# Kernel optimization log

Measured on AMD Instinct MI355X. Metric: run time of the kernel, lower is better.

The kernel has to match this reference:

```python
import jax, jax.numpy as jnp
import numpy as np

CURV = 0.9            # geoopt PoincareBall(0.9)
SQRT_C = CURV ** 0.5
MIN_NORM = 1e-15
PROJ_EPS = 4e-3       # geoopt float32 boundary eps
ATANH_EPS = 1e-7
COS_EPS = 1e-8        # torch.cosine_similarity eps


def _norm(x):
    return jnp.sqrt(jnp.maximum(jnp.sum(x * x, axis=-1, keepdims=True), MIN_NORM * MIN_NORM))


def _project(x):
    # project onto ball of radius (1-eps)/sqrt(c)
    n = jnp.maximum(_norm(x), MIN_NORM)
    maxnorm = (1.0 - PROJ_EPS) / SQRT_C
    return jnp.where(n > maxnorm, x / n * maxnorm, x)


def expmap0(u):
    n = jnp.maximum(_norm(u), MIN_NORM)
    gamma = jnp.tanh(SQRT_C * n) * u / (SQRT_C * n)
    return _project(gamma)


def mobius_add(x, y):
    c = CURV
    x2 = jnp.sum(x * x, axis=-1, keepdims=True)
    y2 = jnp.sum(y * y, axis=-1, keepdims=True)
    xy = jnp.sum(x * y, axis=-1, keepdims=True)
    num = (1.0 + 2.0 * c * xy + c * y2) * x + (1.0 - c * x2) * y
    den = 1.0 + 2.0 * c * xy + c * c * x2 * y2
    return num / jnp.maximum(den, MIN_NORM)


def pdist(x, y):
    # dist(x,y) = 2/sqrt(c) * artanh(sqrt(c) * ||(-x) (+) y||)
    d = mobius_add(-x, y)
    n = _norm(d)[..., 0]
    z = jnp.clip(SQRT_C * n, -1.0 + ATANH_EPS, 1.0 - ATANH_EPS)
    return 2.0 / SQRT_C * jnp.arctanh(z)


def cos_sim(a, b):
    na = jnp.maximum(jnp.sqrt(jnp.sum(a * a, axis=-1)), COS_EPS)
    nb = jnp.maximum(jnp.sqrt(jnp.sum(b * b, axis=-1)), COS_EPS)
    return jnp.sum(a * b, axis=-1) / (na * nb)


def setup_inputs() -> dict:
    key = jax.random.key(0)
    ks = jax.random.split(key, 11)
    B, L, Ls, C, Lc, H, R = 4, 512, 128, 20, 128, 768, 512
    s = 0.02  # keep projected embeddings in a realistic range
    return {
        "text_out": jax.random.normal(ks[0], (B, L, H), jnp.float32),
        "summary_out": jax.random.normal(ks[1], (B, Ls, H), jnp.float32),
        "candidate_out": jax.random.normal(ks[2], (B, C, Lc, H), jnp.float32),
        "W_d": jax.random.normal(ks[3], (H, R), jnp.float32) * s,
        "W_s": jax.random.normal(ks[4], (H, R), jnp.float32) * s,
        "W_c": jax.random.normal(ks[5], (H, R), jnp.float32) * s,
        "W_p": jax.random.normal(ks[6], (R, R), jnp.float32) * s,
        "conv_w1": jax.random.normal(ks[7], (1, H, R), jnp.float32) * s,
        "conv_b1": jax.random.normal(ks[8], (R,), jnp.float32) * s,
        "conv_w2": jax.random.normal(ks[9], (2, H, R), jnp.float32) * s,
        "conv_b2": jax.random.normal(ks[10], (R,), jnp.float32) * s,
    }


def _forward(text_out, summary_out, candidate_out, W_d, W_s, W_c, W_p,
             conv_w1, conv_b1, conv_w2, conv_b2):
    # --- document ---
    doc_emb = expmap0(text_out[:, 0, :] @ W_d)                       # [B,R]

    # NGramers (max_gram=2, eval mode so dropout is identity)
    x = text_out[:, 1:-1, :]                                         # [B,L-2,H]
    y1 = jax.nn.relu(jnp.einsum('blh,hr->blr', x, conv_w1[0]) + conv_b1)
    y2 = jax.nn.relu(jnp.einsum('blh,hr->blr', x[:, :-1], conv_w2[0])
                     + jnp.einsum('blh,hr->blr', x[:, 1:], conv_w2[1]) + conv_b2)
    gram = jnp.concatenate([y1, y2], axis=1)                         # [B,2L-5,R]

    doc_word_emb = expmap0(jnp.einsum('blr,rk->blk', gram, W_p))     # [B,T,R]
    doc_inter = 1.0 / pdist(doc_word_emb, doc_emb[:, None, :])       # [B,T]

    # --- summary ---
    summary_emb = expmap0(jnp.max(summary_out, axis=1) @ W_s)        # [B,R]
    summary_score = -pdist(summary_emb, doc_emb) ** 2                # [B]
    sum_inter = 1.0 / pdist(doc_word_emb, summary_emb[:, None, :])   # [B,T]
    summary_score = summary_score + cos_sim(doc_inter, sum_inter)    # [B]

    # --- candidates ---
    cand_emb = expmap0(jnp.einsum('bch,hr->bcr', jnp.max(candidate_out, axis=2), W_c))  # [B,C,R]
    score = -pdist(cand_emb, doc_emb[:, None, :]) ** 2               # [B,C]
    cand_inter = 1.0 / pdist(doc_word_emb[:, None, :, :], cand_emb[:, :, None, :])      # [B,C,T]
    score = score + cos_sim(doc_inter[:, None, :], cand_inter)       # [B,C]
    return score, summary_score


def reference(text_out, summary_out, candidate_out, W_d, W_s, W_c, W_p,
              conv_w1, conv_b1, conv_w2, conv_b2):
    return _forward(text_out, summary_out, candidate_out, W_d, W_s, W_c, W_p,
                    conv_w1, conv_b1, conv_w2, conv_b2)
```

## Files before the change

### kernel.cpp

```cpp
#include <hip/hip_runtime.h>
#include <math.h>

#define SQRTC  0.94868329805051381f
#define MAXN   (0.996f/SQRTC)
#define OME_CLIP (1.0f - 0.996f*0.996f)
#define TWO_OVER_SQRTC 2.1081851067789197f

typedef unsigned short u16;
typedef __attribute__((ext_vector_type(8))) short bf8;
typedef __attribute__((ext_vector_type(4))) float f4;

__device__ __forceinline__ u16 f2bf(float f){
    union { float f; unsigned int i; } v; v.f = f;
    unsigned int x = v.i;
    unsigned int lsb = (x >> 16) & 1u;
    x += 0x7fffu + lsb;
    return (u16)(x >> 16);
}
__device__ __forceinline__ float bf2f(u16 u){
    union { unsigned int i; float f; } v; v.i = ((unsigned int)u) << 16; return v.f;
}

__device__ __forceinline__ void gload16(void* lds, const void* g){
    __builtin_amdgcn_global_load_lds(
        (const __attribute__((address_space(1))) unsigned int*)g,
        (__attribute__((address_space(3))) unsigned int*)lds,
        16, 0, 0);
}

__device__ __forceinline__ float pdist_stable(float ome_x, float ome_y, float t){
    float u = 1.0f - ome_x, v = 1.0f - ome_y;
    float den = fmaxf(1.0f - 1.8f*t + u*v, 1e-15f);
    float q = ome_x*ome_y/den;
    q = fminf(fmaxf(q, 2.0e-7f), 1.0f);
    float z = sqrtf(fmaxf(1.0f - q, 0.0f));
    float at = 0.5f * logf((1.0f+z)*(1.0f+z)/q);
    return TWO_OVER_SQRTC * at;
}

__device__ __forceinline__ void expmap_scale_ome(float sum, float* fout, float* omeout){
    float nraw = sqrtf(fmaxf(sum, 1e-30f));
    float n = fmaxf(nraw, 1e-15f);
    float sn = SQRTC*n;
    float th = tanhf(sn);
    float factor = th/sn;
    float gn = factor*nraw;
    if (gn > MAXN){ *fout = factor*(MAXN/gn); *omeout = OME_CLIP; }
    else { *fout = factor; *omeout = fmaxf((1.0f-th)*(1.0f+th), 1e-12f); }
}

__global__ __launch_bounds__(256)
void k_stage1(const float* __restrict__ summ, const float* __restrict__ cand,
              const float* __restrict__ text,
              const float* __restrict__ w1, const float* __restrict__ w2,
              const float* __restrict__ wp,
              float* __restrict__ smax, float* __restrict__ cmax,
              u16* __restrict__ textb, u16* __restrict__ w1t,
              u16* __restrict__ w2t, u16* __restrict__ wpt)
{
    __shared__ float shm[1056];
    int bx = blockIdx.x;
    int t = threadIdx.x;
    if (bx < 1008){
        int row = bx / 12, ht = bx - row*12;
        int lane = t & 63, lg = t >> 6;
        int h = ht*64 + lane;
        const float* in = (row < 4) ? (summ + (long long)row*128*768)
                                    : (cand + (long long)(row-4)*128*768);
        const float* p = in + (long long)(lg*32)*768 + h;
        float m = -INFINITY;
        #pragma unroll 8
        for (int l = 0; l < 32; l++) m = fmaxf(m, p[l*768]);
        shm[t] = m; __syncthreads();
        if (t < 64){
            float mm = fmaxf(fmaxf(shm[t], shm[t+64]), fmaxf(shm[t+128], shm[t+192]));
            if (row < 4) smax[row*768 + h] = mm;
            else cmax[(row-4)*768 + h] = mm;
        }
        return;
    }
    int pb = bx - 1008;
    if (pb < 768){
        int base = pb*2048 + t*8;
        float4 a = *(const float4*)(text + base);
        float4 b = *(const float4*)(text + base + 4);
        *(ushort4*)(textb + base)     = make_ushort4(f2bf(a.x), f2bf(a.y), f2bf(a.z), f2bf(a.w));
        *(ushort4*)(textb + base + 4) = make_ushort4(f2bf(b.x), f2bf(b.y), f2bf(b.z), f2bf(b.w));
        return;
    }
    int j = pb - 768;
    const float* in; u16* outp; int K;
    if (j < 384){ in = w1; outp = w1t; K = 768; }
    else if (j < 1152){ j -= 384; in = w2; outp = w2t; K = 1536; }
    else { j -= 1152; in = wp; outp = wpt; K = 512; }
    const int N = 512, ntile = N/32;
    int k0 = (j/ntile)*32, n0 = (j - (j/ntile)*ntile)*32;
    int tx = t & 31, ty = t >> 5;
    #pragma unroll
    for (int i = 0; i < 4; i++)
        shm[(ty*4+i)*33 + tx] = in[(long long)(k0 + ty*4 + i)*N + n0 + tx];
    __syncthreads();
    #pragma unroll
    for (int i = 0; i < 4; i++)
        outp[(long long)(n0 + ty*4 + i)*K + k0 + tx] = f2bf(shm[tx*33 + ty*4+i]);
}

__global__ __launch_bounds__(256)
void k_stage2(const u16* __restrict__ textb,
              const u16* __restrict__ w1t, const u16* __restrict__ w2t,
              const float* __restrict__ cb1, const float* __restrict__ cb2,
              const float* __restrict__ text,
              const float* __restrict__ smax, const float* __restrict__ cmax,
              const float* __restrict__ W_d, const float* __restrict__ W_s,
              const float* __restrict__ W_c,
              u16* __restrict__ gram, float* __restrict__ emb_all)
{
    __shared__ char smem[16384];
    int bx = blockIdx.x;
    int t = threadIdx.x;
    if (bx < 512){
        u16* As = (u16*)smem;
        u16* Bs = (u16*)(smem + 8192);
        int xx = bx & 63, yy = bx >> 6;
        int job = xx & 1;
        int m0 = (xx >> 1) * 64;
        int n0 = yy * 64;
        int K   = job ? 1536 : 768;
        int M   = job ? 2036 : 2040;
        int rpb = job ? 509 : 510;
        int ob  = job ? 510 : 0;
        const u16* Bt = job ? w2t : w1t;
        const float* bias = job ? cb2 : cb1;

        int r0 = t >> 3;
        int co = (((t & 7) ^ (r0 & 7)) << 3);

        int gm0 = m0 + r0;      if (gm0 >= M) gm0 = M - 1;
        int gm1 = m0 + r0 + 32; if (gm1 >= M) gm1 = M - 1;
        int ab0 = gm0 / rpb, al0 = gm0 - ab0*rpb;
        int ab1 = gm1 / rpb, al1 = gm1 - ab1*rpb;
        const u16* a0 = textb + (long long)ab0*393216 + (long long)(al0+1)*768 + co;
        const u16* a1 = textb + (long long)ab1*393216 + (long long)(al1+1)*768 + co;
        const u16* bp0 = Bt + (long long)(n0 + r0)*K      + co;
        const u16* bp1 = Bt + (long long)(n0 + r0 + 32)*K + co;
        u16* lA0 = As + t*8;
        u16* lA1 = As + (256 + t)*8;
        u16* lB0 = Bs + t*8;
        u16* lB1 = Bs + (256 + t)*8;

        int lane = t & 63, wv = t >> 6;
        int fm = lane & 15, fq = lane >> 4;
        int arow = wv*16 + fm;
        int aswz = arow & 7, bswz = fm & 7;
        int aoff0 = arow*64 + ((fq     ^ aswz) << 3);
        int aoff1 = arow*64 + (((4+fq) ^ aswz) << 3);
        int boff0 = ((fq     ^ bswz) << 3);
        int boff1 = (((4+fq) ^ bswz) << 3);

        f4 acc0 = {0,0,0,0}, acc1 = {0,0,0,0}, acc2 = {0,0,0,0}, acc3 = {0,0,0,0};
        for (int k0 = 0; k0 < K; k0 += 64){
            gload16(lA0, a0 + k0);
            gload16(lA1, a1 + k0);
            gload16(lB0, bp0 + k0);
            gload16(lB1, bp1 + k0);
            __syncthreads();
            bf8 af0 = *(const bf8*)(As + aoff0);
            bf8 af1 = *(const bf8*)(As + aoff1);
            bf8 b00 = *(const bf8*)(Bs + (fm   )*64 + boff0);
            bf8 b10 = *(const bf8*)(Bs + (16+fm)*64 + boff0);
            bf8 b20 = *(const bf8*)(Bs + (32+fm)*64 + boff0);
            bf8 b30 = *(const bf8*)(Bs + (48+fm)*64 + boff0);
            bf8 b01 = *(const bf8*)(Bs + (fm   )*64 + boff1);
            bf8 b11 = *(const bf8*)(Bs + (16+fm)*64 + boff1);
            bf8 b21 = *(const bf8*)(Bs + (32+fm)*64 + boff1);
            bf8 b31 = *(const bf8*)(Bs + (48+fm)*64 + boff1);
            acc0 = __builtin_amdgcn_mfma_f32_16x16x32_bf16(af0, b00, acc0, 0, 0, 0);
            acc1 = __builtin_amdgcn_mfma_f32_16x16x32_bf16(af0, b10, acc1, 0, 0, 0);
            acc2 = __builtin_amdgcn_mfma_f32_16x16x32_bf16(af0, b20, acc2, 0, 0, 0);
            acc3 = __builtin_amdgcn_mfma_f32_16x16x32_bf16(af0, b30, acc3, 0, 0, 0);
            acc0 = __builtin_amdgcn_mfma_f32_16x16x32_bf16(af1, b01, acc0, 0, 0, 0);
            acc1 = __builtin_amdgcn_mfma_f32_16x16x32_bf16(af1, b11, acc1, 0, 0, 0);
            acc2 = __builtin_amdgcn_mfma_f32_16x16x32_bf16(af1, b21, acc2, 0, 0, 0);
            acc3 = __builtin_amdgcn_mfma_f32_16x16x32_bf16(af1, b31, acc3, 0, 0, 0);
            __syncthreads();
        }
        int col = n0 + fm;
        float bv0 = bias[col], bv1 = bias[col+16], bv2 = bias[col+32], bv3 = bias[col+48];
        #pragma unroll
        for (int i = 0; i < 4; i++){
            int row = m0 + wv*16 + fq*4 + i;
            if (row >= M) continue;
            int b = row/rpb, l = row - b*rpb;
            long long orow = (long long)b*1019 + ob + l;
            u16* gp = gram + orow*512;
            gp[col]      = f2bf(fmaxf(acc0[i] + bv0, 0.f));
            gp[col + 16] = f2bf(fmaxf(acc1[i] + bv1, 0.f));
            gp[col + 32] = f2bf(fmaxf(acc2[i] + bv2, 0.f));
            gp[col + 48] = f2bf(fmaxf(acc3[i] + bv3, 0.f));
        }
        return;
    }
    {
        int eb = bx - 512;
        int row = eb >> 3, nt = eb & 7;
        float* a   = (float*)smem;
        float* red = (float*)smem + 768;
        const float* A; const float* W;
        if (row < 4){ A = text + (long long)row*512*768; W = W_d; }
        else if (row < 8){ A = smax + (long long)(row-4)*768; W = W_s; }
        else { A = cmax + (long long)(row-8)*768; W = W_c; }
        for (int k = t; k < 768; k += 256) a[k] = A[k];
        __syncthreads();
        int lane = t & 63, kg = t >> 6;
        int col = nt*64 + lane;
        const float* Wp = W + (long long)(kg*192)*512 + col;
        float acc = 0.f;
        #pragma unroll 8
        for (int k = 0; k < 192; k++) acc += a[kg*192 + k] * Wp[k*512];
        red[t] = acc; __syncthreads();
        if (t < 64) emb_all[(long long)row*512 + col] = red[t] + red[t+64] + red[t+128] + red[t+192];
    }
}

__global__ __launch_bounds__(256)
void k_stage3(const u16* __restrict__ gram, const u16* __restrict__ wpt,
              u16* __restrict__ dwe_b,
              float* __restrict__ emb_all, float* __restrict__ ome_all,
              u16* __restrict__ emb_b)
{
    __shared__ char smem[16384];
    int bx = blockIdx.x;
    int t = threadIdx.x;
    if (bx < 512){
        u16* As = (u16*)smem;
        u16* Bs = (u16*)(smem + 8192);
        const int K = 512, M = 4076;
        int m0 = (bx >> 3) * 64;
        int n0 = (bx & 7) * 64;

        int r0 = t >> 3;
        int co = (((t & 7) ^ (r0 & 7)) << 3);
        int gm0 = m0 + r0;      if (gm0 >= M) gm0 = M - 1;
        int gm1 = m0 + r0 + 32; if (gm1 >= M) gm1 = M - 1;
        const u16* a0 = gram + (long long)gm0*512 + co;
        const u16* a1 = gram + (long long)gm1*512 + co;
        const u16* bp0 = wpt + (long long)(n0 + r0)*K      + co;
        const u16* bp1 = wpt + (long long)(n0 + r0 + 32)*K + co;
        u16* lA0 = As + t*8;
        u16* lA1 = As + (256 + t)*8;
        u16* lB0 = Bs + t*8;
        u16* lB1 = Bs + (256 + t)*8;

        int lane = t & 63, wv = t >> 6;
        int fm = lane & 15, fq = lane >> 4;
        int arow = wv*16 + fm;
        int aswz = arow & 7, bswz = fm & 7;
        int aoff0 = arow*64 + ((fq     ^ aswz) << 3);
        int aoff1 = arow*64 + (((4+fq) ^ aswz) << 3);
        int boff0 = ((fq     ^ bswz) << 3);
        int boff1 = (((4+fq) ^ bswz) << 3);

        f4 acc0 = {0,0,0,0}, acc1 = {0,0,0,0}, acc2 = {0,0,0,0}, acc3 = {0,0,0,0};
        for (int k0 = 0; k0 < K; k0 += 64){
            gload16(lA0, a0 + k0);
            gload16(lA1, a1 + k0);
            gload16(lB0, bp0 + k0);
            gload16(lB1, bp1 + k0);
            __syncthreads();
            bf8 af0 = *(const bf8*)(As + aoff0);
            bf8 af1 = *(const bf8*)(As + aoff1);
            bf8 b00 = *(const bf8*)(Bs + (fm   )*64 + boff0);
            bf8 b10 = *(const bf8*)(Bs + (16+fm)*64 + boff0);
            bf8 b20 = *(const bf8*)(Bs + (32+fm)*64 + boff0);
            bf8 b30 = *(const bf8*)(Bs + (48+fm)*64 + boff0);
            bf8 b01 = *(const bf8*)(Bs + (fm   )*64 + boff1);
            bf8 b11 = *(const bf8*)(Bs + (16+fm)*64 + boff1);
            bf8 b21 = *(const bf8*)(Bs + (32+fm)*64 + boff1);
            bf8 b31 = *(const bf8*)(Bs + (48+fm)*64 + boff1);
            acc0 = __builtin_amdgcn_mfma_f32_16x16x32_bf16(af0, b00, acc0, 0, 0, 0);
            acc1 = __builtin_amdgcn_mfma_f32_16x16x32_bf16(af0, b10, acc1, 0, 0, 0);
            acc2 = __builtin_amdgcn_mfma_f32_16x16x32_bf16(af0, b20, acc2, 0, 0, 0);
            acc3 = __builtin_amdgcn_mfma_f32_16x16x32_bf16(af0, b30, acc3, 0, 0, 0);
            acc0 = __builtin_amdgcn_mfma_f32_16x16x32_bf16(af1, b01, acc0, 0, 0, 0);
            acc1 = __builtin_amdgcn_mfma_f32_16x16x32_bf16(af1, b11, acc1, 0, 0, 0);
            acc2 = __builtin_amdgcn_mfma_f32_16x16x32_bf16(af1, b21, acc2, 0, 0, 0);
            acc3 = __builtin_amdgcn_mfma_f32_16x16x32_bf16(af1, b31, acc3, 0, 0, 0);
            __syncthreads();
        }
        int col = n0 + fm;
        #pragma unroll
        for (int i = 0; i < 4; i++){
            int row = m0 + wv*16 + fq*4 + i;
            if (row >= M) continue;
            u16* dp = dwe_b + (long long)row*512;
            dp[col]      = f2bf(acc0[i]);
            dp[col + 16] = f2bf(acc1[i]);
            dp[col + 32] = f2bf(acc2[i]);
            dp[col + 48] = f2bf(acc3[i]);
        }
        return;
    }
    {
        float* red = (float*)smem;
        int row = bx - 512;
        float* X = emb_all + (long long)row*512;
        float2 u = *(float2*)(X + t*2);
        red[t] = u.x*u.x + u.y*u.y; __syncthreads();
        for (int s = 128; s > 0; s >>= 1){ if (t < s) red[t] += red[t+s]; __syncthreads(); }
        float f, ome;
        expmap_scale_ome(red[0], &f, &ome);
        float sx = u.x*f, sy = u.y*f;
        *(float2*)(X + t*2) = make_float2(sx, sy);
        u16* Xb = emb_b + (long long)row*512;
        Xb[t*2]   = f2bf(sx);
        Xb[t*2+1] = f2bf(sy);
        if (t == 0) ome_all[row] = ome;
    }
}

__global__ __launch_bounds__(256)
void k_dots_mfma(const u16* __restrict__ dwe_b, const u16* __restrict__ emb_b,
                 const float* __restrict__ ome_all,
                 float* __restrict__ doc_inter, float* __restrict__ sum_inter,
                 float* __restrict__ cand_inter)
{
    __shared__ u16 As[64][32];
    __shared__ u16 Bs[32][32];
    __shared__ float ssp[64][4];
    __shared__ float ssl[64];
    __shared__ float oyl[22];
    int bx = blockIdx.x;
    int b  = bx >> 4;
    int m0 = (bx & 15) * 64;
    int t = threadIdx.x;
    int sra = t >> 2, ska = (t & 3) << 3;
    const u16* Arow = (m0 + sra < 1019) ? (dwe_b + (long long)(b*1019 + m0 + sra)*512) : nullptr;
    const u16* Brow = nullptr;
    if (t < 128){
        int n = t >> 2;
        if (n < 22){
            int ei = (n == 0) ? b : (n == 1) ? 4 + b : 8 + b*20 + (n - 2);
            Brow = emb_b + (long long)ei*512;
        }
    }
    if (t < 22) oyl[t] = ome_all[(t == 0) ? b : (t == 1) ? 4 + b : 8 + b*20 + (t - 2)];
    int lane = t & 63, wv = t >> 6;
    int fm = lane & 15, fq = lane >> 4;
    f4 acc0 = {0,0,0,0}, acc1 = {0,0,0,0};
    float ssq = 0.f;
    for (int k0 = 0; k0 < 512; k0 += 32){
        bf8 av = {};
        if (Arow) av = *(const bf8*)(Arow + k0 + ska);
        *(bf8*)&As[sra][ska] = av;
        if (t < 128){
            bf8 bv = {};
            if (Brow) bv = *(const bf8*)(Brow + k0 + ((t & 3) << 3));
            *(bf8*)&Bs[t >> 2][(t & 3) << 3] = bv;
        }
        #pragma unroll
        for (int j = 0; j < 8; j++){ float x = bf2f(((u16*)&av)[j]); ssq += x*x; }
        __syncthreads();
        bf8 af = *(const bf8*)&As[wv*16 + fm][fq*8];
        bf8 b0 = *(const bf8*)&Bs[fm][fq*8];
        bf8 b1 = *(const bf8*)&Bs[16 + fm][fq*8];
        acc0 = __builtin_amdgcn_mfma_f32_16x16x32_bf16(af, b0, acc0, 0, 0, 0);
        acc1 = __builtin_amdgcn_mfma_f32_16x16x32_bf16(af, b1, acc1, 0, 0, 0);
        __syncthreads();
    }
    ssp[sra][t & 3] = ssq; __syncthreads();
    if (t < 64) ssl[t] = ssp[t][0] + ssp[t][1] + ssp[t][2] + ssp[t][3];
    __syncthreads();
    #pragma unroll
    for (int i = 0; i < 4; i++){
        int rtile = wv*16 + fq*4 + i;
        int row = m0 + rtile;
        if (row >= 1019) continue;
        float f, ox;
        expmap_scale_ome(ssl[rtile], &f, &ox);
        long long grow = (long long)b*1019 + row;
        #pragma unroll
        for (int g = 0; g < 2; g++){
            int c = g*16 + fm;
            if (c >= 22) continue;
            float s = (g ? acc1[i] : acc0[i]) * f;
            float dist = pdist_stable(ox, oyl[c], s);
            float inv = 1.0f/fmaxf(dist, 1e-12f);
            if (c == 0) doc_inter[grow] = inv;
            else if (c == 1) sum_inter[grow] = inv;
            else cand_inter[((long long)(b*20 + (c - 2)))*1019 + row] = inv;
        }
    }
}

__global__ __launch_bounds__(256)
void k_final(const float* __restrict__ doc_inter, const float* __restrict__ sum_inter,
             const float* __restrict__ cand_inter,
             const float* __restrict__ emb_all, const float* __restrict__ ome_all,
             float* __restrict__ out)
{
    __shared__ float r0[256], r1[256], r2[256], r3[256];
    int j = blockIdx.x, t = threadIdx.x;
    int b; const float *a, *bb; int xi, yi; int outIdx;
    if (j < 80){
        b = j/20;
        a  = doc_inter + b*1019;
        bb = cand_inter + (long long)j*1019;
        xi = 8 + j; yi = b;
        outIdx = j;
    } else {
        b = j - 80;
        a  = doc_inter + b*1019;
        bb = sum_inter + b*1019;
        xi = 4 + b; yi = b;
        outIdx = 80 + b;
    }
    const float* xe = emb_all + (long long)xi*512;
    const float* ye = emb_all + (long long)yi*512;
    float ox = ome_all[xi], oy = ome_all[yi];
    float saa = 0.f, sbb = 0.f, sab = 0.f, st = 0.f;
    for (int l = t; l < 1019; l += 256){ float av = a[l], bv = bb[l]; saa += av*av; sbb += bv*bv; sab += av*bv; }
    for (int k = t; k < 512; k += 256) st += xe[k]*ye[k];
    r0[t] = saa; r1[t] = sbb; r2[t] = sab; r3[t] = st; __syncthreads();
    for (int s = 128; s > 0; s >>= 1){
        if (t < s){ r0[t] += r0[t+s]; r1[t] += r1[t+s]; r2[t] += r2[t+s]; r3[t] += r3[t+s]; }
        __syncthreads();
    }
    if (t == 0){
        float na = fmaxf(sqrtf(r0[0]), 1e-8f);
        float nb = fmaxf(sqrtf(r1[0]), 1e-8f);
        float cosv = r2[0] / (na*nb);
        float pd = pdist_stable(ox, oy, r3[0]);
        out[outIdx] = -pd*pd + cosv;
    }
}

extern "C" void kernel_launch(void* const* d_in, const int* in_sizes, int n_in,
                              void* d_out, int out_size, void* d_ws, size_t ws_size,
                              hipStream_t stream) {
    const float* text = (const float*)d_in[0];
    const float* summ = (const float*)d_in[1];
    const float* cand = (const float*)d_in[2];
    const float* W_d  = (const float*)d_in[3];
    const float* W_s  = (const float*)d_in[4];
    const float* W_c  = (const float*)d_in[5];
    const float* W_p  = (const float*)d_in[6];
    const float* cw1  = (const float*)d_in[7];
    const float* cb1  = (const float*)d_in[8];
    const float* cw2  = (const float*)d_in[9];
    const float* cb2  = (const float*)d_in[10];
    float* out = (float*)d_out;

    const int B = 4, C = 20, H = 768;

    char* base = (char*)d_ws;
    size_t off = 0;
    auto allocF = [&](size_t n)->float*{ float* p = (float*)(base + off); off += ((n*4) + 255) & ~(size_t)255; return p; };
    auto allocU = [&](size_t n)->u16*{ u16* p = (u16*)(base + off); off += ((n*2) + 255) & ~(size_t)255; return p; };

    float* smax = allocF(B*H);
    float* cmax = allocF(B*C*H);
    float* emb_all = allocF(88*512);
    float* ome_all = allocF(88);
    u16* emb_b = allocU(88*512);
    u16* textb = allocU(4*512*768);
    u16* w1t   = allocU(512*768);
    u16* w2t   = allocU(512*1536);
    u16* wpt   = allocU(512*512);
    u16* gram  = allocU(4076*512);
    u16* dwe_b = allocU(4076*512);
    float* doc_inter = allocF(4076);
    float* sum_inter = allocF(4076);
    float* cand_inter= allocF(B*C*1019);

    k_stage1<<<3184, 256, 0, stream>>>(summ, cand, text, cw1, cw2, W_p,
                                       smax, cmax, textb, w1t, w2t, wpt);

    k_stage2<<<1216, 256, 0, stream>>>(textb, w1t, w2t, cb1, cb2,
                                       text, smax, cmax, W_d, W_s, W_c,
                                       gram, emb_all);

    k_stage3<<<600, 256, 0, stream>>>(gram, wpt, dwe_b, emb_all, ome_all, emb_b);

    k_dots_mfma<<<64, 256, 0, stream>>>(dwe_b, emb_b, ome_all,
                                        doc_inter, sum_inter, cand_inter);

    k_final<<<84, 256, 0, stream>>>(doc_inter, sum_inter, cand_inter,
                                    emb_all, ome_all, out);
}
```

Baseline: 150.5 us.

## Vectorize max-pool loads and rework dots kernel into single-wave LDS-free blocks

```diff
diff --git a/kernel.cpp b/kernel.cpp
--- a/kernel.cpp
+++ b/kernel.cpp
@@ -61,25 +61,34 @@
     __shared__ float shm[1056];
     int bx = blockIdx.x;
     int t = threadIdx.x;
-    if (bx < 1008){
-        int row = bx / 12, ht = bx - row*12;
-        int lane = t & 63, lg = t >> 6;
-        int h = ht*64 + lane;
+    if (bx < 252){
+        int row = bx / 3, hc = bx - row*3;
+        int w = t >> 6, lane = t & 63;
         const float* in = (row < 4) ? (summ + (long long)row*128*768)
                                     : (cand + (long long)(row-4)*128*768);
-        const float* p = in + (long long)(lg*32)*768 + h;
-        float m = -INFINITY;
+        const float* p = in + (long long)(w*32)*768 + hc*256 + lane*4;
+        float4 m = make_float4(-INFINITY,-INFINITY,-INFINITY,-INFINITY);
         #pragma unroll 8
-        for (int l = 0; l < 32; l++) m = fmaxf(m, p[l*768]);
-        shm[t] = m; __syncthreads();
+        for (int l = 0; l < 32; l++){
+            float4 v = *(const float4*)(p + (long long)l*768);
+            m.x = fmaxf(m.x, v.x); m.y = fmaxf(m.y, v.y);
+            m.z = fmaxf(m.z, v.z); m.w = fmaxf(m.w, v.w);
+        }
+        float4* sm4 = (float4*)shm;
+        sm4[w*64 + lane] = m; __syncthreads();
         if (t < 64){
-            float mm = fmaxf(fmaxf(shm[t], shm[t+64]), fmaxf(shm[t+128], shm[t+192]));
-            if (row < 4) smax[row*768 + h] = mm;
-            else cmax[(row-4)*768 + h] = mm;
+            float4 a = sm4[t], b4 = sm4[64+t], c4 = sm4[128+t], d4 = sm4[192+t];
+            float4 r;
+            r.x = fmaxf(fmaxf(a.x,b4.x), fmaxf(c4.x,d4.x));
+            r.y = fmaxf(fmaxf(a.y,b4.y), fmaxf(c4.y,d4.y));
+            r.z = fmaxf(fmaxf(a.z,b4.z), fmaxf(c4.z,d4.z));
+            r.w = fmaxf(fmaxf(a.w,b4.w), fmaxf(c4.w,d4.w));
+            float* outp = (row < 4) ? (smax + row*768) : (cmax + (row-4)*768);
+            *(float4*)(outp + hc*256 + t*4) = r;
         }
         return;
     }
-    int pb = bx - 1008;
+    int pb = bx - 252;
     if (pb < 768){
         int base = pb*2048 + t*8;
         float4 a = *(const float4*)(text + base);
@@ -318,76 +327,66 @@
     }
 }
 
-__global__ __launch_bounds__(256)
+__global__ __launch_bounds__(64)
 void k_dots_mfma(const u16* __restrict__ dwe_b, const u16* __restrict__ emb_b,
                  const float* __restrict__ ome_all,
                  float* __restrict__ doc_inter, float* __restrict__ sum_inter,
                  float* __restrict__ cand_inter)
 {
-    __shared__ u16 As[64][32];
-    __shared__ u16 Bs[32][32];
-    __shared__ float ssp[64][4];
-    __shared__ float ssl[64];
-    __shared__ float oyl[22];
     int bx = blockIdx.x;
-    int b  = bx >> 4;
-    int m0 = (bx & 15) * 64;
+    int b  = bx >> 6;
+    int m0 = (bx & 63) * 16;
     int t = threadIdx.x;
-    int sra = t >> 2, ska = (t & 3) << 3;
-    const u16* Arow = (m0 + sra < 1019) ? (dwe_b + (long long)(b*1019 + m0 + sra)*512) : nullptr;
-    const u16* Brow = nullptr;
-    if (t < 128){
-        int n = t >> 2;
-        if (n < 22){
-            int ei = (n == 0) ? b : (n == 1) ? 4 + b : 8 + b*20 + (n - 2);
-            Brow = emb_b + (long long)ei*512;
-        }
-    }
-    if (t < 22) oyl[t] = ome_all[(t == 0) ? b : (t == 1) ? 4 + b : 8 + b*20 + (t - 2)];
-    int lane = t & 63, wv = t >> 6;
-    int fm = lane & 15, fq = lane >> 4;
+    int fm = t & 15, fq = t >> 4;
+
+    int arow = m0 + fm; if (arow > 1018) arow = 1018;
+    const u16* Ap = dwe_b + ((long long)(b*1019 + arow))*512 + fq*8;
+
+    int n1 = 16 + fm; if (n1 > 21) n1 = 21;
+    int e0 = (fm == 0) ? b : (fm == 1) ? 4 + b : 8 + b*20 + (fm - 2);
+    int e1 = 8 + b*20 + (n1 - 2);
+    const u16* B0 = emb_b + (long long)e0*512 + fq*8;
+    const u16* B1 = emb_b + (long long)e1*512 + fq*8;
+    float oy0 = ome_all[e0];
+    float oy1 = ome_all[e1];
+
     f4 acc0 = {0,0,0,0}, acc1 = {0,0,0,0};
     float ssq = 0.f;
+    #pragma unroll 4
     for (int k0 = 0; k0 < 512; k0 += 32){
-        bf8 av = {};
-        if (Arow) av = *(const bf8*)(Arow + k0 + ska);
-        *(bf8*)&As[sra][ska] = av;
-        if (t < 128){
-            bf8 bv = {};
-            if (Brow) bv = *(const bf8*)(Brow + k0 + ((t & 3) << 3));
-            *(bf8*)&Bs[t >> 2][(t & 3) << 3] = bv;
-        }
+        bf8 av  = *(const bf8*)(Ap + k0);
+        bf8 bv0 = *(const bf8*)(B0 + k0);
+        bf8 bv1 = *(const bf8*)(B1 + k0);
         #pragma unroll
         for (int j = 0; j < 8; j++){ float x = bf2f(((u16*)&av)[j]); ssq += x*x; }
-        __syncthreads();
-        bf8 af = *(const bf8*)&As[wv*16 + fm][fq*8];
-        bf8 b0 = *(const bf8*)&Bs[fm][fq*8];
-        bf8 b1 = *(const bf8*)&Bs[16 + fm][fq*8];
-        acc0 = __builtin_amdgcn_mfma_f32_16x16x32_bf16(af, b0, acc0, 0, 0, 0);
-        acc1 = __builtin_amdgcn_mfma_f32_16x16x32_bf16(af, b1, acc1, 0, 0, 0);
-        __syncthreads();
-    }
-    ssp[sra][t & 3] = ssq; __syncthreads();
-    if (t < 64) ssl[t] = ssp[t][0] + ssp[t][1] + ssp[t][2] + ssp[t][3];
-    __syncthreads();
+        acc0 = __builtin_amdgcn_mfma_f32_16x16x32_bf16(av, bv0, acc0, 0, 0, 0);
+        acc1 = __builtin_amdgcn_mfma_f32_16x16x32_bf16(av, bv1, acc1, 0, 0, 0);
+    }
+    ssq += __shfl_xor(ssq, 16);
+    ssq += __shfl_xor(ssq, 32);
+
     #pragma unroll
     for (int i = 0; i < 4; i++){
-        int rtile = wv*16 + fq*4 + i;
-        int row = m0 + rtile;
+        int r = fq*4 + i;
+        float rs = __shfl(ssq, r);
+        int row = m0 + r;
         if (row >= 1019) continue;
         float f, ox;
-        expmap_scale_ome(ssl[rtile], &f, &ox);
+        expmap_scale_ome(rs, &f, &ox);
         long long grow = (long long)b*1019 + row;
-        #pragma unroll
-        for (int g = 0; g < 2; g++){
-            int c = g*16 + fm;
-            if (c >= 22) continue;
-            float s = (g ? acc1[i] : acc0[i]) * f;
-            float dist = pdist_stable(ox, oyl[c], s);
+        {
+            float s = acc0[i] * f;
+            float dist = pdist_stable(ox, oy0, s);
             float inv = 1.0f/fmaxf(dist, 1e-12f);
-            if (c == 0) doc_inter[grow] = inv;
-            else if (c == 1) sum_inter[grow] = inv;
-            else cand_inter[((long long)(b*20 + (c - 2)))*1019 + row] = inv;
+            if (fm == 0) doc_inter[grow] = inv;
+            else if (fm == 1) sum_inter[grow] = inv;
+            else cand_inter[((long long)(b*20 + (fm - 2)))*1019 + row] = inv;
+        }
+        if (16 + fm < 22){
+            float s = acc1[i] * f;
+            float dist = pdist_stable(ox, oy1, s);
+            float inv = 1.0f/fmaxf(dist, 1e-12f);
+            cand_inter[((long long)(b*20 + (16 + fm - 2)))*1019 + row] = inv;
         }
     }
 }
@@ -472,7 +471,7 @@
     float* sum_inter = allocF(4076);
     float* cand_inter= allocF(B*C*1019);
 
-    k_stage1<<<3184, 256, 0, stream>>>(summ, cand, text, cw1, cw2, W_p,
+    k_stage1<<<2428, 256, 0, stream>>>(summ, cand, text, cw1, cw2, W_p,
                                        smax, cmax, textb, w1t, w2t, wpt);
 
     k_stage2<<<1216, 256, 0, stream>>>(textb, w1t, w2t, cb1, cb2,
@@ -481,7 +480,7 @@
 
     k_stage3<<<600, 256, 0, stream>>>(gram, wpt, dwe_b, emb_all, ome_all, emb_b);
 
-    k_dots_mfma<<<64, 256, 0, stream>>>(dwe_b, emb_b, ome_all,
+    k_dots_mfma<<<256, 64, 0, stream>>>(dwe_b, emb_b, ome_all,
                                         doc_inter, sum_inter, cand_inter);
 
     k_final<<<84, 256, 0, stream>>>(doc_inter, sum_inter, cand_inter,
```

After: 141.4 us. 1.06x faster.
